# Performance work log

Hardware: AMD Instinct MI355X
Metric: run time of the kernel (lower is better)

The kernel has to match this reference:

```python
import jax, jax.numpy as jnp
import numpy as np

SEQ, BATCH = 512, 128
FEAT_CH, EMBED = 1024, 1024
N_LANG = 8  # tgt_lang_toks = [0..7]


def setup_inputs() -> dict:
    key = jax.random.key(0)
    k_feat, k_tok, k_w, k_b = jax.random.split(key, 4)
    feat = jax.random.normal(k_feat, (SEQ, BATCH, FEAT_CH), dtype=jnp.float32)
    tgt_lang_toks = jax.random.randint(k_tok, (BATCH,), 0, N_LANG, dtype=jnp.int64)
    # stacked per-language Linear params: W[l] is [embed, feat] (torch Linear layout), b[l] is [embed]
    bound = 1.0 / np.sqrt(FEAT_CH)
    W = jax.random.uniform(k_w, (N_LANG, EMBED, FEAT_CH), minval=-bound, maxval=bound, dtype=jnp.float32)
    b = jax.random.uniform(k_b, (N_LANG, EMBED), minval=-bound, maxval=bound, dtype=jnp.float32)
    return {"feat": feat, "W": W, "b": b, "tgt_lang_toks": tgt_lang_toks}


def reference(feat, W, b, tgt_lang_toks):
    # Each batch column uses the Linear of its language token. Since the
    # language token values equal their index in tgt_lang_toks=[0..7], the
    # per-group mask/gather/scatter of the original collapses to a per-batch
    # weight gather + batched matmul (grouped GEMM as dense dispatch).
    toks = tgt_lang_toks.astype(jnp.int32)
    W_sel = W[toks]          # [B, E, F]
    b_sel = b[toks]          # [B, E]
    # [S,B,F] x [B,E,F] -> [S,B,E]
    out = jnp.einsum('sbf,bef->sbe', feat, W_sel) + b_sel[None, :, :]
    return out
```

## Files before the change

kernel.cpp:

```cpp
#include <hip/hip_runtime.h>
#include <hip/hip_bf16.h>

#define SEQ   512
#define BATCH 128
#define FEAT  1024
#define EMBED 1024
#define NLANG 8

typedef __attribute__((ext_vector_type(8))) short bf16x8;
typedef __attribute__((ext_vector_type(4))) float f32x4;
typedef unsigned short ushort_t;

__device__ __forceinline__ unsigned pk2(float a, float b) {
  float2 f; f.x = a; f.y = b;
  __hip_bfloat162 h = __float22bfloat162_rn(f);
  union { __hip_bfloat162 h2; unsigned u; } cv;
  cv.h2 = h;
  return cv.u;
}

__device__ __forceinline__ void gld16(const void* g, void* l) {
  __builtin_amdgcn_global_load_lds(
      (const __attribute__((address_space(1))) void*)g,
      (__attribute__((address_space(3))) void*)l, 16, 0, 0);
}

__global__ __launch_bounds__(256) void convert_permute_kernel(
    const float* __restrict__ feat,
    const float* __restrict__ Wf,
    const int*   __restrict__ toks,
    ushort_t* __restrict__ Abf,
    ushort_t* __restrict__ Wbf)
{
  __shared__ int stok[128];
  __shared__ int srank[128];
  __shared__ int scnt[8];
  __shared__ int sbase[8];

  const int tid = threadIdx.x;
  if (tid < 128) stok[tid] = toks[tid];
  __syncthreads();
  if (tid < 128) {
    int myt = stok[tid], r = 0;
    for (int j = 0; j < 128; ++j) r += (j < tid) && (stok[j] == myt);
    srank[tid] = r;
  }
  if (tid < 8) {
    int c = 0;
    for (int j = 0; j < 128; ++j) c += (stok[j] == tid);
    scnt[tid] = c;
  }
  __syncthreads();
  if (tid < 8) {
    int b = 0;
    for (int j = 0; j < tid; ++j) b += scnt[j];
    sbase[tid] = b << 9;
  }
  __syncthreads();

  const int FC = (SEQ * BATCH * FEAT) / 4;
  const int TC = FC + (NLANG * EMBED * FEAT) / 4;
  for (int c = blockIdx.x * 256 + tid; c < TC; c += gridDim.x * 256) {
    if (c < FC) {
      float4 v = ((const float4*)feat)[c];
      const int r = c >> 8, q = c & 255;
      const int b = r & 127, s = r >> 7;
      const int tk = stok[b];
      const int p = sbase[tk] + s * scnt[tk] + srank[b];
      uint2 o; o.x = pk2(v.x, v.y); o.y = pk2(v.z, v.w);
      *(uint2*)(Abf + ((size_t)p << 10) + (q << 2)) = o;
    } else {
      const int c2 = c - FC;
      float4 v = ((const float4*)Wf)[c2];
      uint2 o; o.x = pk2(v.x, v.y); o.y = pk2(v.z, v.w);
      *(uint2*)(Wbf + ((size_t)c2 << 2)) = o;
    }
  }
}

__global__ __launch_bounds__(512, 2) void grouped_gemm_pipe(
    const ushort_t* __restrict__ Abf,
    const ushort_t* __restrict__ Wbf,
    const float* __restrict__ bias,
    const int*   __restrict__ toks,
    float*       __restrict__ out)
{
  extern __shared__ ushort_t lds[];
  __shared__ int tokarr[128];
  __shared__ unsigned long long ballots[2][8];
  __shared__ int perm[128];
  __shared__ int rowsrc[256];

  const int tid = threadIdx.x;
  const int l   = tid & 63;
  const int w   = tid >> 6;
  const int wr  = w >> 2;
  const int wc  = w & 3;

  const int bid = blockIdx.x;
  const int L   = (bid & 7) * 128 + (bid >> 3);
  const int et  = L & 3;
  const int mt  = (L >> 7) * 32 + ((L >> 2) & 31);
  const int m0  = mt * 256;
  const int e0  = et * 256;

  if (tid < 128) tokarr[tid] = toks[tid];
  __syncthreads();
  if (tid < 128) {
    int myt = tokarr[tid];
#pragma unroll
    for (int lg = 0; lg < 8; ++lg) {
      unsigned long long bl = __ballot(myt == lg);
      if (l == 0) ballots[w][lg] = bl;
    }
  }
  __syncthreads();

  int lsel = 0, base = 0, csel = 1, boff_sel = 0;
  {
    int cum = 0, boff = 0;
#pragma unroll
    for (int lg = 0; lg < 8; ++lg) {
      int c = __popcll(ballots[0][lg]) + __popcll(ballots[1][lg]);
      int seg = c << 9;
      bool in = (m0 >= cum) && (m0 < cum + seg);
      if (in) { lsel = lg; base = cum; csel = c; boff_sel = boff; }
      cum += seg; boff += c;
    }
  }

  if (tid < 128) {
    int myt = tokarr[tid];
    unsigned long long ltm = (1ull << l) - 1ull;
    int rank = (w == 0) ? __popcll(ballots[0][myt] & ltm)
                        : __popcll(ballots[0][myt]) + __popcll(ballots[1][myt] & ltm);
    int boff2 = 0;
#pragma unroll
    for (int lg = 0; lg < 8; ++lg) {
      int c = __popcll(ballots[0][lg]) + __popcll(ballots[1][lg]);
      boff2 += (lg < myt) ? c : 0;
    }
    perm[boff2 + rank] = tid;
  }
  __syncthreads();
  if (tid < 256) {
    int local = m0 - base + tid;
    int s = local / csel;
    int j = local - s * csel;
    rowsrc[tid] = s * BATCH + perm[boff_sel + j];
  }
  __syncthreads();

  const int ca   = w * 128 + l;
  const int rwA  = ca >> 2;
  const int ccA  = ca & 3;
  const int sA   = (rwA >> 1) & 3;
  const ushort_t* aS0 = Abf + (size_t)(m0 + rwA) * FEAT + ((ccA ^ sA) * 8);
  const ushort_t* aS1 = aS0 + (size_t)16 * FEAT;
  const ushort_t* bS0 = Wbf + ((size_t)lsel * EMBED + e0 + rwA) * FEAT + ((ccA ^ sA) * 8);
  const ushort_t* bS1 = bS0 + (size_t)16 * FEAT;
  const int dOff0 = (w * 128) * 8;
  const int dOff1 = (w * 128 + 64) * 8;

  const int kc  = l >> 4;
  const int rA  = wr * 128 + (l & 15);
  const int aRd = rA * 32 + ((kc ^ ((rA >> 1) & 3)) * 8);
  const int rB  = wc * 64 + (l & 15);
  const int bRd = rB * 32 + ((kc ^ ((rB >> 1) & 3)) * 8);

  f32x4 acc[8][4] = {};

#define STAGE(kt, buf)                                                     \
  do {                                                                     \
    const int _o = (kt) * 32;                                              \
    gld16(aS0 + _o, lds + (buf) * 8192 + dOff0);                           \
    gld16(aS1 + _o, lds + (buf) * 8192 + dOff1);                           \
    gld16(bS0 + _o, lds + 32768 + (buf) * 8192 + dOff0);                   \
    gld16(bS1 + _o, lds + 32768 + (buf) * 8192 + dOff1);                   \
  } while (0)

  STAGE(0, 0);
  STAGE(1, 1);
  STAGE(2, 2);
  asm volatile("s_waitcnt vmcnt(8)" ::: "memory");
  __builtin_amdgcn_s_barrier();
  __builtin_amdgcn_sched_barrier(0);

  const int NT = FEAT / 32;
  for (int t = 0; t < NT; ++t) {
    const ushort_t* Ab = lds + (t & 3) * 8192;
    const ushort_t* Bb = lds + 32768 + (t & 3) * 8192;
    if (t < NT - 3) STAGE(t + 3, (t + 3) & 3);

    bf16x8 af[8], bfq[4];
#pragma unroll
    for (int mf = 0; mf < 8; ++mf)
      af[mf] = *(const bf16x8*)(Ab + aRd + mf * 512);
#pragma unroll
    for (int nf = 0; nf < 4; ++nf)
      bfq[nf] = *(const bf16x8*)(Bb + bRd + nf * 512);

    __builtin_amdgcn_s_setprio(1);
#pragma unroll
    for (int mf = 0; mf < 8; ++mf)
#pragma unroll
      for (int nf = 0; nf < 4; ++nf)
        acc[mf][nf] = __builtin_amdgcn_mfma_f32_16x16x32_bf16(
            af[mf], bfq[nf], acc[mf][nf], 0, 0, 0);
    __builtin_amdgcn_s_setprio(0);

    if (t < NT - 3)       asm volatile("s_waitcnt vmcnt(8)" ::: "memory");
    else if (t == NT - 3) asm volatile("s_waitcnt vmcnt(4)" ::: "memory");
    else if (t == NT - 2) asm volatile("s_waitcnt vmcnt(0)" ::: "memory");
    if (t < NT - 1) {
      __builtin_amdgcn_s_barrier();
      __builtin_amdgcn_sched_barrier(0);
    }
  }
#undef STAGE

  const int col = l & 15;
  const int r4  = (l >> 4) * 4;
  float bvv[4];
#pragma unroll
  for (int nf = 0; nf < 4; ++nf)
    bvv[nf] = bias[lsel * EMBED + e0 + wc * 64 + nf * 16 + col];
#pragma unroll
  for (int mf = 0; mf < 8; ++mf) {
#pragma unroll
    for (int j = 0; j < 4; ++j) {
      const size_t ro = (size_t)rowsrc[wr * 128 + mf * 16 + r4 + j] * EMBED;
#pragma unroll
      for (int nf = 0; nf < 4; ++nf)
        out[ro + e0 + wc * 64 + nf * 16 + col] = acc[mf][nf][j] + bvv[nf];
    }
  }
}

__global__ __launch_bounds__(256, 2) void grouped_proj_fused(
    const float* __restrict__ feat, const float* __restrict__ Wt,
    const float* __restrict__ bias, const int* __restrict__ toks,
    float* __restrict__ out)
{
  __shared__ uint4 As[1024];
  __shared__ uint4 Bs[1024];
  __shared__ int tokarr[128];
  __shared__ unsigned long long ballots[2][8];
  __shared__ int perm[128];
  __shared__ int rowsrc[128];

  const int tid  = threadIdx.x;
  const int lane = tid & 63;
  const int wv   = tid >> 6;
  const int wr   = wv >> 1;
  const int wc   = wv & 1;
  const int bid = blockIdx.x;
  const int xcd = bid & 7;
  const int sq  = bid >> 3;
  const int et  = sq & 7;
  const int mt  = (sq >> 3) * 8 + xcd;
  const int m0  = mt * 128;
  const int e0  = et * 128;

  if (tid < 128) tokarr[tid] = toks[tid];
  __syncthreads();
  if (tid < 128) {
    int myt = tokarr[tid];
#pragma unroll
    for (int lg = 0; lg < 8; ++lg) {
      unsigned long long bl = __ballot(myt == lg);
      if (lane == 0) ballots[wv][lg] = bl;
    }
  }
  __syncthreads();
  int lsel = 0, base = 0, csel = 1, boff_sel = 0;
  {
    int cum = 0, boff = 0;
#pragma unroll
    for (int lg = 0; lg < 8; ++lg) {
      int c = __popcll(ballots[0][lg]) + __popcll(ballots[1][lg]);
      int seg = c << 9;
      bool in = (m0 >= cum) && (m0 < cum + seg);
      if (in) { lsel = lg; base = cum; csel = c; boff_sel = boff; }
      cum += seg; boff += c;
    }
  }
  if (tid < 128) {
    int myt = tokarr[tid];
    unsigned long long ltm = (1ull << lane) - 1ull;
    int rank = (wv == 0) ? __popcll(ballots[0][myt] & ltm)
                         : __popcll(ballots[0][myt]) + __popcll(ballots[1][myt] & ltm);
    int boff2 = 0;
#pragma unroll
    for (int lg = 0; lg < 8; ++lg) {
      int c = __popcll(ballots[0][lg]) + __popcll(ballots[1][lg]);
      boff2 += (lg < myt) ? c : 0;
    }
    perm[boff2 + rank] = tid;
  }
  __syncthreads();
  if (tid < 128) {
    int local = m0 - base + tid;
    int s = local / csel;
    int j = local - s * csel;
    rowsrc[tid] = s * BATCH + perm[boff_sel + j];
  }
  __syncthreads();

  int slot_i[4];
  const float* aptr[4];
  const float* bptr[4];
#pragma unroll
  for (int it = 0; it < 4; ++it) {
    int c    = it * 256 + tid;
    int kg   = c & 7;
    int row  = c >> 3;
    int ksub = kg & 3;
    int kk   = kg >> 2;
    int frag = row >> 4;
    slot_i[it] = (kk * 8 + frag) * 64 + ((row & 15) ^ (ksub << 1) ^ kk) + ksub * 16;
    aptr[it] = feat + (size_t)rowsrc[row] * FEAT + kg * 8;
    bptr[it] = Wt + ((size_t)lsel * EMBED + e0 + row) * FEAT + kg * 8;
  }

  f32x4 acc[4][4] = {};
  for (int k0 = 0; k0 < FEAT; k0 += 64) {
    __syncthreads();
#pragma unroll
    for (int it = 0; it < 4; ++it) {
      float4 alo = *(const float4*)(aptr[it] + k0);
      float4 ahi = *(const float4*)(aptr[it] + k0 + 4);
      uint4 av;
      av.x = pk2(alo.x, alo.y); av.y = pk2(alo.z, alo.w);
      av.z = pk2(ahi.x, ahi.y); av.w = pk2(ahi.z, ahi.w);
      As[slot_i[it]] = av;
      float4 blo = *(const float4*)(bptr[it] + k0);
      float4 bhi = *(const float4*)(bptr[it] + k0 + 4);
      uint4 bv;
      bv.x = pk2(blo.x, blo.y); bv.y = pk2(blo.z, blo.w);
      bv.z = pk2(bhi.x, bhi.y); bv.w = pk2(bhi.z, bhi.w);
      Bs[slot_i[it]] = bv;
    }
    __syncthreads();
#pragma unroll
    for (int kk = 0; kk < 2; ++kk) {
      const int ksr = lane >> 4;
      const int sw  = ((lane & 15) ^ (ksr << 1) ^ kk) + ksr * 16;
      bf16x8 af[4], bfr[4];
#pragma unroll
      for (int mi = 0; mi < 4; ++mi)
        af[mi] = ((const bf16x8*)As)[(kk * 8 + wr * 4 + mi) * 64 + sw];
#pragma unroll
      for (int ni = 0; ni < 4; ++ni)
        bfr[ni] = ((const bf16x8*)Bs)[(kk * 8 + wc * 4 + ni) * 64 + sw];
#pragma unroll
      for (int mi = 0; mi < 4; ++mi)
#pragma unroll
        for (int ni = 0; ni < 4; ++ni)
          acc[mi][ni] = __builtin_amdgcn_mfma_f32_16x16x32_bf16(
              af[mi], bfr[ni], acc[mi][ni], 0, 0, 0);
    }
  }

  const int col = lane & 15;
  const int r0  = (lane >> 4) * 4;
  float bvv[4];
#pragma unroll
  for (int ni = 0; ni < 4; ++ni)
    bvv[ni] = bias[lsel * EMBED + e0 + wc * 64 + ni * 16 + col];
#pragma unroll
  for (int mi = 0; mi < 4; ++mi) {
#pragma unroll
    for (int j = 0; j < 4; ++j) {
      const size_t ro = (size_t)rowsrc[wr * 64 + mi * 16 + r0 + j] * EMBED;
#pragma unroll
      for (int ni = 0; ni < 4; ++ni)
        out[ro + e0 + wc * 64 + ni * 16 + col] = acc[mi][ni][j] + bvv[ni];
    }
  }
}

extern "C" void kernel_launch(void* const* d_in, const int* in_sizes, int n_in,
                              void* d_out, int out_size, void* d_ws, size_t ws_size,
                              hipStream_t stream) {
  const float* feat = (const float*)d_in[0];
  const float* W    = (const float*)d_in[1];
  const float* bias = (const float*)d_in[2];
  const int*   toks = (const int*)d_in[3];
  float* out = (float*)d_out;

  const size_t abf_bytes = (size_t)SEQ * BATCH * FEAT * 2;
  const size_t wbf_bytes = (size_t)NLANG * EMBED * FEAT * 2;

  if (ws_size >= abf_bytes + wbf_bytes) {
    ushort_t* Abf = (ushort_t*)d_ws;
    ushort_t* Wbf = (ushort_t*)((char*)d_ws + abf_bytes);
    convert_permute_kernel<<<3072, 256, 0, stream>>>(feat, W, toks, Abf, Wbf);
    (void)hipFuncSetAttribute((const void*)grouped_gemm_pipe,
                              hipFuncAttributeMaxDynamicSharedMemorySize, 131072);
    const int nblk = (SEQ * BATCH / 256) * (EMBED / 256);
    grouped_gemm_pipe<<<nblk, 512, 131072, stream>>>(Abf, Wbf, bias, toks, out);
  } else {
    grouped_proj_fused<<<(SEQ * BATCH / 128) * (EMBED / 128), 256, 0, stream>>>(
        feat, W, bias, toks, out);
  }
}
```

Baseline: 261.9 us.

## Split GEMM main loop into two interleaved phases with barrier-synced MFMA clusters

Restructures the K-loop of the grouped bf16 GEMM so that each K-step runs in two phases. Each phase issues half the LDS fragment reads and half the global-to-LDS prefetches (A in the first phase, B in the second), then runs a cluster of MFMAs on the upper or lower half of the M fragments. Barriers around each cluster keep waves in lockstep, in the style of ping-pong scheduling. The goal is finer interleaving of memory and matrix work and fewer fragment registers held at once, at the cost of twice as many workgroup barriers per K-step.

```diff
diff --git a/kernel.cpp b/kernel.cpp
--- a/kernel.cpp
+++ b/kernel.cpp
@@ -78,7 +78,7 @@
   }
 }
 
-__global__ __launch_bounds__(512, 2) void grouped_gemm_pipe(
+__global__ __launch_bounds__(512, 2) void grouped_gemm_8ph(
     const ushort_t* __restrict__ Abf,
     const ushort_t* __restrict__ Wbf,
     const float* __restrict__ bias,
@@ -169,55 +169,78 @@
   const int bRd = rB * 32 + ((kc ^ ((rB >> 1) & 3)) * 8);
 
   f32x4 acc[8][4] = {};
-
-#define STAGE(kt, buf)                                                     \
+  bf16x8 af0[4], af1[4], bfq[4];
+
+#define STAGE_A(kt, buf)                                                   \
+  do { const int _o = (kt) * 32;                                           \
+    gld16(aS0 + _o, lds + (buf) * 8192 + dOff0);                           \
+    gld16(aS1 + _o, lds + (buf) * 8192 + dOff1); } while (0)
+#define STAGE_B(kt, buf)                                                   \
+  do { const int _o = (kt) * 32;                                           \
+    gld16(bS0 + _o, lds + 32768 + (buf) * 8192 + dOff0);                   \
+    gld16(bS1 + _o, lds + 32768 + (buf) * 8192 + dOff1); } while (0)
+
+#define PH0(g, DOSTAGE)                                                    \
   do {                                                                     \
-    const int _o = (kt) * 32;                                              \
-    gld16(aS0 + _o, lds + (buf) * 8192 + dOff0);                           \
-    gld16(aS1 + _o, lds + (buf) * 8192 + dOff1);                           \
-    gld16(bS0 + _o, lds + 32768 + (buf) * 8192 + dOff0);                   \
-    gld16(bS1 + _o, lds + 32768 + (buf) * 8192 + dOff1);                   \
+    const ushort_t* Ab_ = lds + ((g) & 3) * 8192;                          \
+    const ushort_t* Bb_ = lds + 32768 + ((g) & 3) * 8192;                  \
+    _Pragma("unroll") for (int mf = 0; mf < 4; ++mf)                       \
+        af0[mf] = *(const bf16x8*)(Ab_ + aRd + mf * 512);                  \
+    _Pragma("unroll") for (int nf = 0; nf < 4; ++nf)                       \
+        bfq[nf] = *(const bf16x8*)(Bb_ + bRd + nf * 512);                  \
+    if (DOSTAGE) { STAGE_A((g) + 3, ((g) + 3) & 3); }                      \
+    __builtin_amdgcn_sched_barrier(0);                                     \
+    __builtin_amdgcn_s_barrier();                                          \
+    asm volatile("s_waitcnt lgkmcnt(0)" ::: "memory");                     \
+    __builtin_amdgcn_sched_barrier(0);                                     \
+    __builtin_amdgcn_s_setprio(1);                                         \
+    _Pragma("unroll") for (int mf = 0; mf < 4; ++mf)                       \
+        _Pragma("unroll") for (int nf = 0; nf < 4; ++nf)                   \
+            acc[mf][nf] = __builtin_amdgcn_mfma_f32_16x16x32_bf16(         \
+                af0[mf], bfq[nf], acc[mf][nf], 0, 0, 0);                   \
+    __builtin_amdgcn_s_setprio(0);                                         \
+    __builtin_amdgcn_s_barrier();                                          \
   } while (0)
 
-  STAGE(0, 0);
-  STAGE(1, 1);
-  STAGE(2, 2);
+#define PH1(g, DOSTAGE, WAIT)                                              \
+  do {                                                                     \
+    const ushort_t* Ab_ = lds + ((g) & 3) * 8192;                          \
+    _Pragma("unroll") for (int mf = 0; mf < 4; ++mf)                       \
+        af1[mf] = *(const bf16x8*)(Ab_ + aRd + (mf + 4) * 512);            \
+    if (DOSTAGE) { STAGE_B((g) + 3, ((g) + 3) & 3); }                      \
+    __builtin_amdgcn_sched_barrier(0);                                     \
+    __builtin_amdgcn_s_barrier();                                          \
+    asm volatile("s_waitcnt lgkmcnt(0)" ::: "memory");                     \
+    __builtin_amdgcn_sched_barrier(0);                                     \
+    __builtin_amdgcn_s_setprio(1);                                         \
+    _Pragma("unroll") for (int mf = 0; mf < 4; ++mf)                       \
+        _Pragma("unroll") for (int nf = 0; nf < 4; ++nf)                   \
+            acc[mf + 4][nf] = __builtin_amdgcn_mfma_f32_16x16x32_bf16(     \
+                af1[mf], bfq[nf], acc[mf + 4][nf], 0, 0, 0);               \
+    __builtin_amdgcn_s_setprio(0);                                         \
+    asm volatile(WAIT ::: "memory");                                       \
+    __builtin_amdgcn_s_barrier();                                          \
+  } while (0)
+
+  STAGE_A(0, 0); STAGE_B(0, 0);
+  STAGE_A(1, 1); STAGE_B(1, 1);
+  STAGE_A(2, 2); STAGE_B(2, 2);
   asm volatile("s_waitcnt vmcnt(8)" ::: "memory");
   __builtin_amdgcn_s_barrier();
   __builtin_amdgcn_sched_barrier(0);
 
-  const int NT = FEAT / 32;
-  for (int t = 0; t < NT; ++t) {
-    const ushort_t* Ab = lds + (t & 3) * 8192;
-    const ushort_t* Bb = lds + 32768 + (t & 3) * 8192;
-    if (t < NT - 3) STAGE(t + 3, (t + 3) & 3);
-
-    bf16x8 af[8], bfq[4];
-#pragma unroll
-    for (int mf = 0; mf < 8; ++mf)
-      af[mf] = *(const bf16x8*)(Ab + aRd + mf * 512);
-#pragma unroll
-    for (int nf = 0; nf < 4; ++nf)
-      bfq[nf] = *(const bf16x8*)(Bb + bRd + nf * 512);
-
-    __builtin_amdgcn_s_setprio(1);
-#pragma unroll
-    for (int mf = 0; mf < 8; ++mf)
-#pragma unroll
-      for (int nf = 0; nf < 4; ++nf)
-        acc[mf][nf] = __builtin_amdgcn_mfma_f32_16x16x32_bf16(
-            af[mf], bfq[nf], acc[mf][nf], 0, 0, 0);
-    __builtin_amdgcn_s_setprio(0);
-
-    if (t < NT - 3)       asm volatile("s_waitcnt vmcnt(8)" ::: "memory");
-    else if (t == NT - 3) asm volatile("s_waitcnt vmcnt(4)" ::: "memory");
-    else if (t == NT - 2) asm volatile("s_waitcnt vmcnt(0)" ::: "memory");
-    if (t < NT - 1) {
-      __builtin_amdgcn_s_barrier();
-      __builtin_amdgcn_sched_barrier(0);
-    }
-  }
-#undef STAGE
+  for (int g = 0; g < 29; ++g) {
+    PH0(g, true);
+    PH1(g, true, "s_waitcnt vmcnt(8)");
+  }
+  PH0(29, false); PH1(29, false, "s_waitcnt vmcnt(4)");
+  PH0(30, false); PH1(30, false, "s_waitcnt vmcnt(0)");
+  PH0(31, false); PH1(31, false, "s_nop 0");
+
+#undef PH0
+#undef PH1
+#undef STAGE_A
+#undef STAGE_B
 
   const int col = l & 15;
   const int r4  = (l >> 4) * 4;
@@ -396,10 +419,10 @@
     ushort_t* Abf = (ushort_t*)d_ws;
     ushort_t* Wbf = (ushort_t*)((char*)d_ws + abf_bytes);
     convert_permute_kernel<<<3072, 256, 0, stream>>>(feat, W, toks, Abf, Wbf);
-    (void)hipFuncSetAttribute((const void*)grouped_gemm_pipe,
+    (void)hipFuncSetAttribute((const void*)grouped_gemm_8ph,
                               hipFuncAttributeMaxDynamicSharedMemorySize, 131072);
     const int nblk = (SEQ * BATCH / 256) * (EMBED / 256);
-    grouped_gemm_pipe<<<nblk, 512, 131072, stream>>>(Abf, Wbf, bias, toks, out);
+    grouped_gemm_8ph<<<nblk, 512, 131072, stream>>>(Abf, Wbf, bias, toks, out);
   } else {
     grouped_proj_fused<<<(SEQ * BATCH / 128) * (EMBED / 128), 256, 0, stream>>>(
         feat, W, bias, toks, out);
```

Result: no change. 260.7 us (-0.5%).
